# Kernel optimization log

Measured on AMD Instinct MI355X. Metric: run time of the kernel, lower is better.

Reference implementation:

```python
import jax, jax.numpy as jnp
import numpy as np

B, R, N = 4, 1024, 100
REG_FG_THRESH = 0.55
EPS = 1e-8


def _cross2(a, b):
    return a[..., 0] * b[..., 1] - a[..., 1] * b[..., 0]


def _corners_bev(box):
    # box: (7,) [x,y,z,dx,dy,dz,heading] -> (4,2) CCW BEV corners
    x, y, dx, dy, ang = box[0], box[1], box[3], box[4], box[6]
    c, s = jnp.cos(ang), jnp.sin(ang)
    lx = jnp.array([0.5, -0.5, -0.5, 0.5], dtype=box.dtype) * dx
    ly = jnp.array([0.5, 0.5, -0.5, -0.5], dtype=box.dtype) * dy
    return jnp.stack([x + lx * c - ly * s, y + lx * s + ly * c], axis=-1)


def _points_in_box(pts, box):
    # pts (P,2), box (7,) -> (P,) bool; transform into box frame
    c, s = jnp.cos(box[6]), jnp.sin(box[6])
    px = pts[:, 0] - box[0]
    py = pts[:, 1] - box[1]
    lx = px * c + py * s
    ly = -px * s + py * c
    return (jnp.abs(lx) <= box[3] * 0.5 + 1e-5) & (jnp.abs(ly) <= box[4] * 0.5 + 1e-5)


def _bev_inter_area(boxa, boxb):
    # exact rotated-rectangle intersection area (convex polygon of <=8 verts)
    ca = _corners_bev(boxa)
    cb = _corners_bev(boxb)
    in_b = _points_in_box(ca, boxb)
    in_a = _points_in_box(cb, boxa)
    a1, a2 = ca, jnp.roll(ca, -1, axis=0)
    b1, b2 = cb, jnp.roll(cb, -1, axis=0)
    d1 = a2 - a1
    d2 = b2 - b1
    denom = _cross2(d1[:, None, :], d2[None, :, :])              # (4,4)
    diff = b1[None, :, :] - a1[:, None, :]                       # (4,4,2)
    safe = jnp.where(jnp.abs(denom) > EPS, denom, EPS)
    t = _cross2(diff, d2[None, :, :]) / safe
    u = _cross2(diff, d1[:, None, :]) / safe
    hit = (jnp.abs(denom) > EPS) & (t >= 0) & (t <= 1) & (u >= 0) & (u <= 1)
    pin = a1[:, None, :] + t[..., None] * d1[:, None, :]         # (4,4,2)
    pts = jnp.concatenate([ca, cb, pin.reshape(16, 2)], axis=0)  # (24,2)
    val = jnp.concatenate([in_b, in_a, hit.reshape(16)], axis=0)
    nv = val.sum()
    ctr = (pts * val[:, None]).sum(0) / jnp.maximum(nv, 1)
    ang = jnp.where(val, jnp.arctan2(pts[:, 1] - ctr[1], pts[:, 0] - ctr[0]), 1e9)
    order = jnp.argsort(ang)
    p = pts[order]
    v = val[order]
    first = p[0]
    p = jnp.where(v[:, None], p, first)   # pad invalid slots with first vertex (zero shoelace contribution)
    q = jnp.roll(p, -1, axis=0)
    area = 0.5 * jnp.abs(jnp.sum(p[:, 0] * q[:, 1] - q[:, 0] * p[:, 1]))
    return jnp.where(nv >= 3, area, jnp.zeros((), dtype=pts.dtype))


def _iou3d_pair(a, b):
    # same math as iou3d_nms_utils.boxes_iou3d_gpu for one pair
    inter_bev = _bev_inter_area(a, b)
    oh = jnp.clip(jnp.minimum(a[2] + a[5] * 0.5, b[2] + b[5] * 0.5)
                  - jnp.maximum(a[2] - a[5] * 0.5, b[2] - b[5] * 0.5), 0.0)
    inter = inter_bev * oh
    va = a[3] * a[4] * a[5]
    vb = b[3] * b[4] * b[5]
    return inter / jnp.clip(va + vb - inter, 1e-6, None)


_iou_rois_gts = jax.vmap(jax.vmap(_iou3d_pair, in_axes=(None, 0)), in_axes=(0, None))  # (R,N)
_iou_batched = jax.vmap(_iou_rois_gts)                                                  # (B,R,N)


def setup_inputs() -> dict:
    key = jax.random.key(0)
    ks = jax.random.split(key, 9)
    xy = jax.random.uniform(ks[0], (B, N, 2), minval=-40.0, maxval=40.0)
    z = jax.random.uniform(ks[1], (B, N, 1), minval=-2.0, maxval=0.0)
    dims = jax.random.uniform(ks[2], (B, N, 3), minval=1.0, maxval=4.5)
    heading = jax.random.uniform(ks[3], (B, N, 1), minval=-np.pi, maxval=np.pi)
    labels = jax.random.randint(ks[4], (B, N, 1), 1, 4).astype(jnp.float32)
    gt_boxes = jnp.concatenate([xy, z, dims, heading, labels], axis=-1)  # (B,N,8)
    # sampling ROIs are jittered GT boxes, mirroring generate_sampling_roi
    base_idx = jax.random.randint(ks[5], (B, R), 0, N)
    base = jnp.take_along_axis(gt_boxes[..., :7], base_idx[..., None], axis=1)  # (B,R,7)
    ctr_off = jax.random.uniform(ks[6], (B, R, 3), minval=-0.5, maxval=0.5) * base[..., 3:6]
    scale = jax.random.uniform(ks[7], (B, R, 3), minval=0.8, maxval=1.25)
    ang_off = jax.random.uniform(ks[8], (B, R, 1), minval=-np.pi / 4, maxval=np.pi / 4)
    sampling_rois = jnp.concatenate(
        [base[..., :3] + ctr_off, base[..., 3:6] * scale, base[..., 6:7] + ang_off], axis=-1)
    sampling_rois_labels = jnp.take_along_axis(gt_boxes[..., 7], base_idx, axis=1).astype(jnp.int32)
    return {"sampling_rois": sampling_rois,
            "sampling_rois_labels": sampling_rois_labels,
            "gt_boxes": gt_boxes}


def reference(sampling_rois, sampling_rois_labels, gt_boxes):
    # sample_rois_for_rcnn core: all-pairs rotated 3D IoU, best-GT assignment,
    # gather gt_of_rois, then forward()'s reg_valid_mask thresholding.
    iou3d = _iou_batched(sampling_rois, gt_boxes[..., :7])        # (B,R,N)
    max_overlaps = iou3d.max(axis=-1)                             # (B,R)
    gt_assignment = iou3d.argmax(axis=-1)                         # (B,R)
    gt_of_rois = jnp.take_along_axis(gt_boxes, gt_assignment[..., None], axis=1)  # (B,R,8)
    reg_valid_mask = (max_overlaps > REG_FG_THRESH).astype(jnp.int32)
    return sampling_rois, gt_of_rois, max_overlaps, sampling_rois_labels, reg_valid_mask
```

## Files before the change

kernel.cpp:

```cpp
#include <hip/hip_runtime.h>
#include <math.h>

#define BB 4
#define RR 1024
#define NN 100
#define NROI (BB * RR)
#define RPB 2
#define PPB (RPB * NN)
#define NBLK (NROI / RPB)

#define INIT_PACK 0x00000000FFFFFFFFull

__device__ __forceinline__ void corner_of(int i, float cx0, float cy0, float dx, float dy,
                                          float c, float s, float& X, float& Y) {
    float sx = (i == 0 || i == 3) ? 0.5f : -0.5f;
    float sy = (i <= 1) ? 0.5f : -0.5f;
    float lx = sx * dx, ly = sy * dy;
    X = cx0 + lx * c - ly * s;
    Y = cy0 + lx * s + ly * c;
}

__global__ __launch_bounds__(256) void sampling_target_fused(
    const float* __restrict__ rois,
    const int*   __restrict__ labels,
    const float* __restrict__ gts,
    float*       __restrict__ out)
{
    __shared__ int   s_list[PPB];
    __shared__ int   s_cnt;
    __shared__ unsigned long long s_best[RPB];

    const int tid = threadIdx.x;
    const int roi0 = blockIdx.x * RPB;
    const int b = roi0 >> 10;

    if (tid < RPB) s_best[tid] = INIT_PACK;
    if (tid == 0) s_cnt = 0;
    __syncthreads();

    {
        bool hit = false;
        const int p = tid;
        if (p < PPB) {
            int rl = p / NN;
            int n = p - rl * NN;
            const float* A = &rois[(roi0 + rl) * 7];
            const float* G = &gts[(b * NN + n) * 8];
            float oh = fminf(A[2] + A[5] * 0.5f, G[2] + G[5] * 0.5f)
                     - fmaxf(A[2] - A[5] * 0.5f, G[2] - G[5] * 0.5f);
            float dxc = A[0] - G[0], dyc = A[1] - G[1];
            float ra = 0.5f * sqrtf(A[3] * A[3] + A[4] * A[4]);
            float rb = 0.5f * sqrtf(G[3] * G[3] + G[4] * G[4]);
            float rr = ra + rb;
            hit = (oh > 0.0f) && (dxc * dxc + dyc * dyc <= rr * rr);
        }
        unsigned long long m = __ballot(hit);
        int wl = tid & 63;
        int nh = __popcll(m);
        if (nh) {
            int base = 0;
            if (wl == 0) base = atomicAdd(&s_cnt, nh);
            base = __shfl(base, 0, 64);
            if (hit) {
                int pfx = __popcll(m & ((1ull << wl) - 1ull));
                s_list[base + pfx] = p;
            }
        }
    }
    __syncthreads();

    const int cnt = s_cnt;
    const int g = tid >> 5;
    const int lane = tid & 31;
    const int half = g & 1;

    for (int i = g; i < cnt; i += 8) {
        int p = s_list[i];
        int rl = p / NN;
        int n = p - rl * NN;
        const float* A = &rois[(roi0 + rl) * 7];
        const float* G = &gts[(b * NN + n) * 8];
        float ax = A[0], ay = A[1], az = A[2], adx = A[3], ady = A[4], adz = A[5], aang = A[6];
        float gx_ = G[0], gy_ = G[1], gz_ = G[2], gdx = G[3], gdy = G[4], gdz = G[5], gang = G[6];
        float acs = cosf(aang), asn = sinf(aang);
        float bcs = cosf(gang), bsn = sinf(gang);

        float ppx = 0.0f, ppy = 0.0f;
        bool val = false;
        if (lane < 4) {
            corner_of(lane, ax, ay, adx, ady, acs, asn, ppx, ppy);
            float qx = ppx - gx_, qy = ppy - gy_;
            float lx = qx * bcs + qy * bsn;
            float ly = -qx * bsn + qy * bcs;
            val = (fabsf(lx) <= gdx * 0.5f + 1e-5f) && (fabsf(ly) <= gdy * 0.5f + 1e-5f);
        } else if (lane < 8) {
            corner_of(lane - 4, gx_, gy_, gdx, gdy, bcs, bsn, ppx, ppy);
            float qx = ppx - ax, qy = ppy - ay;
            float lx = qx * acs + qy * asn;
            float ly = -qx * asn + qy * acs;
            val = (fabsf(lx) <= adx * 0.5f + 1e-5f) && (fabsf(ly) <= ady * 0.5f + 1e-5f);
        } else if (lane < 24) {
            int e = lane - 8;
            int ii = e >> 2, jj = e & 3;
            float a1x, a1y, a2x, a2y, b1x, b1y, b2x, b2y;
            corner_of(ii, ax, ay, adx, ady, acs, asn, a1x, a1y);
            corner_of((ii + 1) & 3, ax, ay, adx, ady, acs, asn, a2x, a2y);
            corner_of(jj, gx_, gy_, gdx, gdy, bcs, bsn, b1x, b1y);
            corner_of((jj + 1) & 3, gx_, gy_, gdx, gdy, bcs, bsn, b2x, b2y);
            float d1x = a2x - a1x, d1y = a2y - a1y;
            float d2x = b2x - b1x, d2y = b2y - b1y;
            float denom = d1x * d2y - d1y * d2x;
            float fx = b1x - a1x, fy = b1y - a1y;
            float safe = (fabsf(denom) > 1e-8f) ? denom : 1e-8f;
            float t = (fx * d2y - fy * d2x) / safe;
            float u = (fx * d1y - fy * d1x) / safe;
            ppx = a1x + t * d1x;
            ppy = a1y + t * d1y;
            val = (fabsf(denom) > 1e-8f) && (t >= 0.0f) && (t <= 1.0f) && (u >= 0.0f) && (u <= 1.0f);
        }

        unsigned long long m = __ballot(val);
        unsigned gm = (unsigned)(half ? (m >> 32) : (m & 0xFFFFFFFFull));
        int nv = __popc(gm);

        float inter_bev = 0.0f;
        if (nv >= 3) {
            float sx = val ? ppx : 0.0f;
            float sy = val ? ppy : 0.0f;
#pragma unroll
            for (int off = 16; off; off >>= 1) {
                sx += __shfl_xor(sx, off, 32);
                sy += __shfl_xor(sy, off, 32);
            }
            float cx = sx / (float)nv, cy = sy / (float)nv;

            float dxp = ppx - cx, dyp = ppy - cy;
            float den = fabsf(dxp) + fabsf(dyp);
            float pa = dxp / fmaxf(den, 1e-30f);
            float myAng = val ? copysignf(1.0f - pa, dyp) : 1e9f;

            float sAng = 1e30f; int sIdx = 0; bool found = false;
            float gAng = 1e30f; int gIdx = 0;
#pragma unroll
            for (int j = 0; j < 24; j++) {
                float aj = __shfl(myAng, j, 32);
                if (aj < 1e8f) {
                    bool greater = (aj > myAng) || (aj == myAng && j > lane);
                    if (greater && aj < sAng) { sAng = aj; sIdx = j; found = true; }
                    if (aj < gAng) { gAng = aj; gIdx = j; }
                }
            }
            int qi = found ? sIdx : gIdx;
            float qx = __shfl(ppx, qi, 32);
            float qy = __shfl(ppy, qi, 32);
            float contrib = val ? (ppx * qy - qx * ppy) : 0.0f;
#pragma unroll
            for (int off = 16; off; off >>= 1)
                contrib += __shfl_xor(contrib, off, 32);
            inter_bev = 0.5f * fabsf(contrib);
        }

        if (lane == 0) {
            float oh = fminf(az + adz * 0.5f, gz_ + gdz * 0.5f)
                     - fmaxf(az - adz * 0.5f, gz_ - gdz * 0.5f);
            float inter = inter_bev * oh;
            float va = adx * ady * adz;
            float vb = gdx * gdy * gdz;
            float v = inter / fmaxf(va + vb - inter, 1e-6f);
            unsigned long long packed =
                ((unsigned long long)__float_as_uint(v) << 32) | (unsigned)(~(unsigned)n);
            atomicMax(&s_best[rl], packed);
        }
    }
    __syncthreads();

    if (tid < RPB) {
        int r = roi0 + tid;
        unsigned long long packed = s_best[tid];
        float mo = __uint_as_float((unsigned)(packed >> 32));
        int besti = (int)(~(unsigned)(packed & 0xFFFFFFFFu));

        const float* Ar = &rois[r * 7];
        const float* Gb = &gts[(b * NN + besti) * 8];

        float* out_rois = out;
        float* out_gor  = out + NROI * 7;
        float* out_max  = out_gor + NROI * 8;
        float* out_lab  = out_max + NROI;
        float* out_msk  = out_lab + NROI;

#pragma unroll
        for (int k = 0; k < 7; k++) out_rois[r * 7 + k] = Ar[k];
#pragma unroll
        for (int k = 0; k < 8; k++) out_gor[r * 8 + k] = Gb[k];
        out_max[r] = mo;
        out_lab[r] = (float)labels[r];
        out_msk[r] = (mo > 0.55f) ? 1.0f : 0.0f;
    }
}

extern "C" void kernel_launch(void* const* d_in, const int* in_sizes, int n_in,
                              void* d_out, int out_size, void* d_ws, size_t ws_size,
                              hipStream_t stream) {
    const float* rois   = (const float*)d_in[0];
    const int*   labels = (const int*)d_in[1];
    const float* gts    = (const float*)d_in[2];
    float* out = (float*)d_out;

    hipLaunchKernelGGL(sampling_target_fused, dim3(NBLK), dim3(256), 0, stream,
                       rois, labels, gts, out);
}
```

Baseline: 70.32 us.

## Stage GT and ROI boxes with precomputed trig in shared memory, four ROIs per block

Each block now loads the batch's 100 GT boxes and its ROIs into shared memory once, precomputing cos/sin and the circumradius per box. The per-pair prefilter and exact-IoU loops read from LDS instead of repeatedly loading from global memory and recomputing the trig. ROIs per block go from 2 to 4 so the GT staging is shared across more work, with the prefilter looping over the 400 pairs. This halves the block count and adds per-block setup and shared memory use, which reduces parallelism.

```diff
diff --git a/kernel.cpp b/kernel.cpp
--- a/kernel.cpp
+++ b/kernel.cpp
@@ -5,7 +5,7 @@
 #define RR 1024
 #define NN 100
 #define NROI (BB * RR)
-#define RPB 2
+#define RPB 4
 #define PPB (RPB * NN)
 #define NBLK (NROI / RPB)
 
@@ -26,6 +26,10 @@
     const float* __restrict__ gts,
     float*       __restrict__ out)
 {
+    __shared__ float s_gx[NN], s_gy[NN], s_gz[NN], s_gdx[NN], s_gdy[NN], s_gdz[NN],
+                     s_gang[NN], s_glab[NN], s_gc[NN], s_gs[NN], s_grb[NN];
+    __shared__ float s_rx[RPB], s_ry[RPB], s_rz[RPB], s_rdx[RPB], s_rdy[RPB], s_rdz[RPB],
+                     s_rang[RPB], s_rc[RPB], s_rs[RPB], s_rra[RPB];
     __shared__ int   s_list[PPB];
     __shared__ int   s_cnt;
     __shared__ unsigned long long s_best[RPB];
@@ -34,24 +38,39 @@
     const int roi0 = blockIdx.x * RPB;
     const int b = roi0 >> 10;
 
+    if (tid < NN) {
+        const float4* G = (const float4*)&gts[(b * NN + tid) * 8];
+        float4 g0 = G[0];
+        float4 g1 = G[1];
+        s_gx[tid] = g0.x;  s_gy[tid] = g0.y;  s_gz[tid] = g0.z;  s_gdx[tid] = g0.w;
+        s_gdy[tid] = g1.x; s_gdz[tid] = g1.y; s_gang[tid] = g1.z; s_glab[tid] = g1.w;
+        s_gc[tid] = cosf(g1.z);
+        s_gs[tid] = sinf(g1.z);
+        s_grb[tid] = 0.5f * sqrtf(g0.w * g0.w + g1.x * g1.x);
+    } else if (tid < NN + RPB) {
+        int rl = tid - NN;
+        const float* A = &rois[(roi0 + rl) * 7];
+        float ax = A[0], ay = A[1], az = A[2], adx = A[3], ady = A[4], adz = A[5], aang = A[6];
+        s_rx[rl] = ax; s_ry[rl] = ay; s_rz[rl] = az;
+        s_rdx[rl] = adx; s_rdy[rl] = ady; s_rdz[rl] = adz; s_rang[rl] = aang;
+        s_rc[rl] = cosf(aang);
+        s_rs[rl] = sinf(aang);
+        s_rra[rl] = 0.5f * sqrtf(adx * adx + ady * ady);
+    }
     if (tid < RPB) s_best[tid] = INIT_PACK;
     if (tid == 0) s_cnt = 0;
     __syncthreads();
 
-    {
+    for (int p0 = 0; p0 < PPB; p0 += 256) {
+        int p = p0 + tid;
         bool hit = false;
-        const int p = tid;
         if (p < PPB) {
             int rl = p / NN;
             int n = p - rl * NN;
-            const float* A = &rois[(roi0 + rl) * 7];
-            const float* G = &gts[(b * NN + n) * 8];
-            float oh = fminf(A[2] + A[5] * 0.5f, G[2] + G[5] * 0.5f)
-                     - fmaxf(A[2] - A[5] * 0.5f, G[2] - G[5] * 0.5f);
-            float dxc = A[0] - G[0], dyc = A[1] - G[1];
-            float ra = 0.5f * sqrtf(A[3] * A[3] + A[4] * A[4]);
-            float rb = 0.5f * sqrtf(G[3] * G[3] + G[4] * G[4]);
-            float rr = ra + rb;
+            float oh = fminf(s_rz[rl] + s_rdz[rl] * 0.5f, s_gz[n] + s_gdz[n] * 0.5f)
+                     - fmaxf(s_rz[rl] - s_rdz[rl] * 0.5f, s_gz[n] - s_gdz[n] * 0.5f);
+            float dxc = s_rx[rl] - s_gx[n], dyc = s_ry[rl] - s_gy[n];
+            float rr = s_rra[rl] + s_grb[n];
             hit = (oh > 0.0f) && (dxc * dxc + dyc * dyc <= rr * rr);
         }
         unsigned long long m = __ballot(hit);
@@ -78,12 +97,12 @@
         int p = s_list[i];
         int rl = p / NN;
         int n = p - rl * NN;
-        const float* A = &rois[(roi0 + rl) * 7];
-        const float* G = &gts[(b * NN + n) * 8];
-        float ax = A[0], ay = A[1], az = A[2], adx = A[3], ady = A[4], adz = A[5], aang = A[6];
-        float gx_ = G[0], gy_ = G[1], gz_ = G[2], gdx = G[3], gdy = G[4], gdz = G[5], gang = G[6];
-        float acs = cosf(aang), asn = sinf(aang);
-        float bcs = cosf(gang), bsn = sinf(gang);
+        float ax = s_rx[rl], ay = s_ry[rl], az = s_rz[rl];
+        float adx = s_rdx[rl], ady = s_rdy[rl], adz = s_rdz[rl];
+        float acs = s_rc[rl], asn = s_rs[rl];
+        float gx_ = s_gx[n], gy_ = s_gy[n], gz_ = s_gz[n];
+        float gdx = s_gdx[n], gdy = s_gdy[n], gdz = s_gdz[n];
+        float bcs = s_gc[n], bsn = s_gs[n];
 
         float ppx = 0.0f, ppy = 0.0f;
         bool val = false;
@@ -180,19 +199,29 @@
         float mo = __uint_as_float((unsigned)(packed >> 32));
         int besti = (int)(~(unsigned)(packed & 0xFFFFFFFFu));
 
-        const float* Ar = &rois[r * 7];
-        const float* Gb = &gts[(b * NN + besti) * 8];
-
         float* out_rois = out;
         float* out_gor  = out + NROI * 7;
         float* out_max  = out_gor + NROI * 8;
         float* out_lab  = out_max + NROI;
         float* out_msk  = out_lab + NROI;
 
-#pragma unroll
-        for (int k = 0; k < 7; k++) out_rois[r * 7 + k] = Ar[k];
-#pragma unroll
-        for (int k = 0; k < 8; k++) out_gor[r * 8 + k] = Gb[k];
+        out_rois[r * 7 + 0] = s_rx[tid];
+        out_rois[r * 7 + 1] = s_ry[tid];
+        out_rois[r * 7 + 2] = s_rz[tid];
+        out_rois[r * 7 + 3] = s_rdx[tid];
+        out_rois[r * 7 + 4] = s_rdy[tid];
+        out_rois[r * 7 + 5] = s_rdz[tid];
+        out_rois[r * 7 + 6] = s_rang[tid];
+
+        out_gor[r * 8 + 0] = s_gx[besti];
+        out_gor[r * 8 + 1] = s_gy[besti];
+        out_gor[r * 8 + 2] = s_gz[besti];
+        out_gor[r * 8 + 3] = s_gdx[besti];
+        out_gor[r * 8 + 4] = s_gdy[besti];
+        out_gor[r * 8 + 5] = s_gdz[besti];
+        out_gor[r * 8 + 6] = s_gang[besti];
+        out_gor[r * 8 + 7] = s_glab[besti];
+
         out_max[r] = mo;
         out_lab[r] = (float)labels[r];
         out_msk[r] = (mo > 0.55f) ? 1.0f : 0.0f;
```

Measured after the change: 66.26 us. 5.8% less time.

## Assign fixed ROI-half per warp group and iterate hit GTs via ballot bitmask

Applied to the files above, without the earlier changes.

Each 32-lane group now owns one ROI and half of the GT boxes, running the cheap prefilter per lane and then looping over hit bits with shuffles to broadcast GT parameters. This removes the shared-memory hit list, its atomics and one block barrier, and keeps the best IoU in registers instead of using a shared atomicMax. ROIs per block rise from two to four, and GT loads and output copies use float4 accesses. The trade-off is load imbalance between groups, since each group's loop length depends on its own hit count, plus serialized shuffle broadcasts per candidate.

```diff
diff --git a/kernel.cpp b/kernel.cpp
--- a/kernel.cpp
+++ b/kernel.cpp
@@ -5,8 +5,7 @@
 #define RR 1024
 #define NN 100
 #define NROI (BB * RR)
-#define RPB 2
-#define PPB (RPB * NN)
+#define RPB 4
 #define NBLK (NROI / RPB)
 
 #define INIT_PACK 0x00000000FFFFFFFFull
@@ -26,176 +25,178 @@
     const float* __restrict__ gts,
     float*       __restrict__ out)
 {
-    __shared__ int   s_list[PPB];
-    __shared__ int   s_cnt;
-    __shared__ unsigned long long s_best[RPB];
-
-    const int tid = threadIdx.x;
+    __shared__ unsigned long long s_best[8];
+
+    const int tid  = threadIdx.x;
     const int roi0 = blockIdx.x * RPB;
-    const int b = roi0 >> 10;
-
-    if (tid < RPB) s_best[tid] = INIT_PACK;
-    if (tid == 0) s_cnt = 0;
-    __syncthreads();
-
-    {
-        bool hit = false;
-        const int p = tid;
-        if (p < PPB) {
-            int rl = p / NN;
-            int n = p - rl * NN;
-            const float* A = &rois[(roi0 + rl) * 7];
-            const float* G = &gts[(b * NN + n) * 8];
-            float oh = fminf(A[2] + A[5] * 0.5f, G[2] + G[5] * 0.5f)
-                     - fmaxf(A[2] - A[5] * 0.5f, G[2] - G[5] * 0.5f);
-            float dxc = A[0] - G[0], dyc = A[1] - G[1];
-            float ra = 0.5f * sqrtf(A[3] * A[3] + A[4] * A[4]);
-            float rb = 0.5f * sqrtf(G[3] * G[3] + G[4] * G[4]);
-            float rr = ra + rb;
-            hit = (oh > 0.0f) && (dxc * dxc + dyc * dyc <= rr * rr);
-        }
-        unsigned long long m = __ballot(hit);
-        int wl = tid & 63;
-        int nh = __popcll(m);
-        if (nh) {
-            int base = 0;
-            if (wl == 0) base = atomicAdd(&s_cnt, nh);
-            base = __shfl(base, 0, 64);
-            if (hit) {
-                int pfx = __popcll(m & ((1ull << wl) - 1ull));
-                s_list[base + pfx] = p;
-            }
-        }
-    }
-    __syncthreads();
-
-    const int cnt = s_cnt;
-    const int g = tid >> 5;
+    const int b    = roi0 >> 10;
+    const int g    = tid >> 5;
     const int lane = tid & 31;
     const int half = g & 1;
-
-    for (int i = g; i < cnt; i += 8) {
-        int p = s_list[i];
-        int rl = p / NN;
-        int n = p - rl * NN;
-        const float* A = &rois[(roi0 + rl) * 7];
-        const float* G = &gts[(b * NN + n) * 8];
-        float ax = A[0], ay = A[1], az = A[2], adx = A[3], ady = A[4], adz = A[5], aang = A[6];
-        float gx_ = G[0], gy_ = G[1], gz_ = G[2], gdx = G[3], gdy = G[4], gdz = G[5], gang = G[6];
-        float acs = cosf(aang), asn = sinf(aang);
-        float bcs = cosf(gang), bsn = sinf(gang);
-
-        float ppx = 0.0f, ppy = 0.0f;
-        bool val = false;
-        if (lane < 4) {
-            corner_of(lane, ax, ay, adx, ady, acs, asn, ppx, ppy);
-            float qx = ppx - gx_, qy = ppy - gy_;
-            float lx = qx * bcs + qy * bsn;
-            float ly = -qx * bsn + qy * bcs;
-            val = (fabsf(lx) <= gdx * 0.5f + 1e-5f) && (fabsf(ly) <= gdy * 0.5f + 1e-5f);
-        } else if (lane < 8) {
-            corner_of(lane - 4, gx_, gy_, gdx, gdy, bcs, bsn, ppx, ppy);
-            float qx = ppx - ax, qy = ppy - ay;
-            float lx = qx * acs + qy * asn;
-            float ly = -qx * asn + qy * acs;
-            val = (fabsf(lx) <= adx * 0.5f + 1e-5f) && (fabsf(ly) <= ady * 0.5f + 1e-5f);
-        } else if (lane < 24) {
-            int e = lane - 8;
-            int ii = e >> 2, jj = e & 3;
-            float a1x, a1y, a2x, a2y, b1x, b1y, b2x, b2y;
-            corner_of(ii, ax, ay, adx, ady, acs, asn, a1x, a1y);
-            corner_of((ii + 1) & 3, ax, ay, adx, ady, acs, asn, a2x, a2y);
-            corner_of(jj, gx_, gy_, gdx, gdy, bcs, bsn, b1x, b1y);
-            corner_of((jj + 1) & 3, gx_, gy_, gdx, gdy, bcs, bsn, b2x, b2y);
-            float d1x = a2x - a1x, d1y = a2y - a1y;
-            float d2x = b2x - b1x, d2y = b2y - b1y;
-            float denom = d1x * d2y - d1y * d2x;
-            float fx = b1x - a1x, fy = b1y - a1y;
-            float safe = (fabsf(denom) > 1e-8f) ? denom : 1e-8f;
-            float t = (fx * d2y - fy * d2x) / safe;
-            float u = (fx * d1y - fy * d1x) / safe;
-            ppx = a1x + t * d1x;
-            ppy = a1y + t * d1y;
-            val = (fabsf(denom) > 1e-8f) && (t >= 0.0f) && (t <= 1.0f) && (u >= 0.0f) && (u <= 1.0f);
+    const int rl   = g >> 1;
+    const int h    = g & 1;
+    const int r    = roi0 + rl;
+
+    const float* A = &rois[r * 7];
+    float ax = A[0], ay = A[1], az = A[2], adx = A[3], ady = A[4], adz = A[5], aang = A[6];
+    float acs = cosf(aang), asn = sinf(aang);
+    float ra  = 0.5f * sqrtf(adx * adx + ady * ady);
+    float azl = az - adz * 0.5f, azh = az + adz * 0.5f;
+    float va  = adx * ady * adz;
+
+    unsigned long long best = INIT_PACK;
+
+    for (int r2 = 0; r2 < 2; ++r2) {
+        int local = r2 * 32 + lane;
+        int n     = h * 50 + local;
+        bool valid = (local < 50);
+
+        float4 g0 = make_float4(0.f, 0.f, 0.f, 0.f);
+        float4 g1 = make_float4(0.f, 0.f, 0.f, 0.f);
+        if (valid) {
+            const float4* G = (const float4*)&gts[(b * NN + n) * 8];
+            g0 = G[0];
+            g1 = G[1];
         }
-
-        unsigned long long m = __ballot(val);
+        float gc = cosf(g1.z), gs = sinf(g1.z);
+
+        float ohz = fminf(azh, g0.z + g1.y * 0.5f) - fmaxf(azl, g0.z - g1.y * 0.5f);
+        float dxc = ax - g0.x, dyc = ay - g0.y;
+        float rsum = ra + 0.5f * sqrtf(g0.w * g0.w + g1.x * g1.x);
+        bool hit = valid && (ohz > 0.0f) && (dxc * dxc + dyc * dyc <= rsum * rsum);
+
+        unsigned long long m = __ballot(hit);
         unsigned gm = (unsigned)(half ? (m >> 32) : (m & 0xFFFFFFFFull));
-        int nv = __popc(gm);
-
-        float inter_bev = 0.0f;
-        if (nv >= 3) {
-            float sx = val ? ppx : 0.0f;
-            float sy = val ? ppy : 0.0f;
+
+        while (gm) {
+            int j = __ffs(gm) - 1;
+            gm &= gm - 1;
+
+            float gx_ = __shfl(g0.x, j, 32);
+            float gy_ = __shfl(g0.y, j, 32);
+            float gz_ = __shfl(g0.z, j, 32);
+            float gdx = __shfl(g0.w, j, 32);
+            float gdy = __shfl(g1.x, j, 32);
+            float gdz = __shfl(g1.y, j, 32);
+            float bcs = __shfl(gc, j, 32);
+            float bsn = __shfl(gs, j, 32);
+            int   nj  = h * 50 + r2 * 32 + j;
+
+            float ppx = 0.0f, ppy = 0.0f;
+            bool val = false;
+            if (lane < 4) {
+                corner_of(lane, ax, ay, adx, ady, acs, asn, ppx, ppy);
+                float qx = ppx - gx_, qy = ppy - gy_;
+                float lx = qx * bcs + qy * bsn;
+                float ly = -qx * bsn + qy * bcs;
+                val = (fabsf(lx) <= gdx * 0.5f + 1e-5f) && (fabsf(ly) <= gdy * 0.5f + 1e-5f);
+            } else if (lane < 8) {
+                corner_of(lane - 4, gx_, gy_, gdx, gdy, bcs, bsn, ppx, ppy);
+                float qx = ppx - ax, qy = ppy - ay;
+                float lx = qx * acs + qy * asn;
+                float ly = -qx * asn + qy * acs;
+                val = (fabsf(lx) <= adx * 0.5f + 1e-5f) && (fabsf(ly) <= ady * 0.5f + 1e-5f);
+            } else if (lane < 24) {
+                int e = lane - 8;
+                int ii = e >> 2, jj = e & 3;
+                float a1x, a1y, a2x, a2y, b1x, b1y, b2x, b2y;
+                corner_of(ii, ax, ay, adx, ady, acs, asn, a1x, a1y);
+                corner_of((ii + 1) & 3, ax, ay, adx, ady, acs, asn, a2x, a2y);
+                corner_of(jj, gx_, gy_, gdx, gdy, bcs, bsn, b1x, b1y);
+                corner_of((jj + 1) & 3, gx_, gy_, gdx, gdy, bcs, bsn, b2x, b2y);
+                float d1x = a2x - a1x, d1y = a2y - a1y;
+                float d2x = b2x - b1x, d2y = b2y - b1y;
+                float denom = d1x * d2y - d1y * d2x;
+                float fx = b1x - a1x, fy = b1y - a1y;
+                float safe = (fabsf(denom) > 1e-8f) ? denom : 1e-8f;
+                float t = (fx * d2y - fy * d2x) / safe;
+                float u = (fx * d1y - fy * d1x) / safe;
+                ppx = a1x + t * d1x;
+                ppy = a1y + t * d1y;
+                val = (fabsf(denom) > 1e-8f) && (t >= 0.0f) && (t <= 1.0f) && (u >= 0.0f) && (u <= 1.0f);
+            }
+
+            unsigned long long mv = __ballot(val);
+            unsigned gv = (unsigned)(half ? (mv >> 32) : (mv & 0xFFFFFFFFull));
+            int nv = __popc(gv);
+
+            float inter_bev = 0.0f;
+            if (nv >= 3) {
+                float sx = val ? ppx : 0.0f;
+                float sy = val ? ppy : 0.0f;
 #pragma unroll
-            for (int off = 16; off; off >>= 1) {
-                sx += __shfl_xor(sx, off, 32);
-                sy += __shfl_xor(sy, off, 32);
+                for (int off = 16; off; off >>= 1) {
+                    sx += __shfl_xor(sx, off, 32);
+                    sy += __shfl_xor(sy, off, 32);
+                }
+                float cx = sx / (float)nv, cy = sy / (float)nv;
+
+                float dxp = ppx - cx, dyp = ppy - cy;
+                float den = fabsf(dxp) + fabsf(dyp);
+                float pa = dxp / fmaxf(den, 1e-30f);
+                float myAng = val ? copysignf(1.0f - pa, dyp) : 1e9f;
+
+                float sAng = 1e30f; int sIdx = 0; bool found = false;
+                float gAng = 1e30f; int gIdx = 0;
+#pragma unroll
+                for (int jx = 0; jx < 24; jx++) {
+                    float aj = __shfl(myAng, jx, 32);
+                    if (aj < 1e8f) {
+                        bool greater = (aj > myAng) || (aj == myAng && jx > lane);
+                        if (greater && aj < sAng) { sAng = aj; sIdx = jx; found = true; }
+                        if (aj < gAng) { gAng = aj; gIdx = jx; }
+                    }
+                }
+                int qi = found ? sIdx : gIdx;
+                float qx = __shfl(ppx, qi, 32);
+                float qy = __shfl(ppy, qi, 32);
+                float contrib = val ? (ppx * qy - qx * ppy) : 0.0f;
+#pragma unroll
+                for (int off = 16; off; off >>= 1)
+                    contrib += __shfl_xor(contrib, off, 32);
+                inter_bev = 0.5f * fabsf(contrib);
             }
-            float cx = sx / (float)nv, cy = sy / (float)nv;
-
-            float dxp = ppx - cx, dyp = ppy - cy;
-            float den = fabsf(dxp) + fabsf(dyp);
-            float pa = dxp / fmaxf(den, 1e-30f);
-            float myAng = val ? copysignf(1.0f - pa, dyp) : 1e9f;
-
-            float sAng = 1e30f; int sIdx = 0; bool found = false;
-            float gAng = 1e30f; int gIdx = 0;
-#pragma unroll
-            for (int j = 0; j < 24; j++) {
-                float aj = __shfl(myAng, j, 32);
-                if (aj < 1e8f) {
-                    bool greater = (aj > myAng) || (aj == myAng && j > lane);
-                    if (greater && aj < sAng) { sAng = aj; sIdx = j; found = true; }
-                    if (aj < gAng) { gAng = aj; gIdx = j; }
-                }
-            }
-            int qi = found ? sIdx : gIdx;
-            float qx = __shfl(ppx, qi, 32);
-            float qy = __shfl(ppy, qi, 32);
-            float contrib = val ? (ppx * qy - qx * ppy) : 0.0f;
-#pragma unroll
-            for (int off = 16; off; off >>= 1)
-                contrib += __shfl_xor(contrib, off, 32);
-            inter_bev = 0.5f * fabsf(contrib);
-        }
-
-        if (lane == 0) {
-            float oh = fminf(az + adz * 0.5f, gz_ + gdz * 0.5f)
-                     - fmaxf(az - adz * 0.5f, gz_ - gdz * 0.5f);
-            float inter = inter_bev * oh;
-            float va = adx * ady * adz;
+
+            float ohp = fminf(azh, gz_ + gdz * 0.5f) - fmaxf(azl, gz_ - gdz * 0.5f);
+            float inter = inter_bev * ohp;
             float vb = gdx * gdy * gdz;
             float v = inter / fmaxf(va + vb - inter, 1e-6f);
             unsigned long long packed =
-                ((unsigned long long)__float_as_uint(v) << 32) | (unsigned)(~(unsigned)n);
-            atomicMax(&s_best[rl], packed);
+                ((unsigned long long)__float_as_uint(v) << 32) | (unsigned)(~(unsigned)nj);
+            best = (packed > best) ? packed : best;
         }
     }
+
+    if (lane == 0) s_best[g] = best;
     __syncthreads();
 
+    float* out_rois = out;
+    float* out_gor  = out + NROI * 7;
+    float* out_max  = out_gor + NROI * 8;
+    float* out_lab  = out_max + NROI;
+    float* out_msk  = out_lab + NROI;
+
+    if (tid < RPB * 7)
+        out_rois[roi0 * 7 + tid] = rois[roi0 * 7 + tid];
+
     if (tid < RPB) {
-        int r = roi0 + tid;
-        unsigned long long packed = s_best[tid];
+        unsigned long long p0 = s_best[2 * tid];
+        unsigned long long p1 = s_best[2 * tid + 1];
+        unsigned long long packed = (p0 > p1) ? p0 : p1;
         float mo = __uint_as_float((unsigned)(packed >> 32));
         int besti = (int)(~(unsigned)(packed & 0xFFFFFFFFu));
 
-        const float* Ar = &rois[r * 7];
-        const float* Gb = &gts[(b * NN + besti) * 8];
-
-        float* out_rois = out;
-        float* out_gor  = out + NROI * 7;
-        float* out_max  = out_gor + NROI * 8;
-        float* out_lab  = out_max + NROI;
-        float* out_msk  = out_lab + NROI;
-
-#pragma unroll
-        for (int k = 0; k < 7; k++) out_rois[r * 7 + k] = Ar[k];
-#pragma unroll
-        for (int k = 0; k < 8; k++) out_gor[r * 8 + k] = Gb[k];
-        out_max[r] = mo;
-        out_lab[r] = (float)labels[r];
-        out_msk[r] = (mo > 0.55f) ? 1.0f : 0.0f;
+        int rr_ = roi0 + tid;
+        const float4* G = (const float4*)&gts[(b * NN + besti) * 8];
+        float4 q0 = G[0];
+        float4 q1 = G[1];
+        float4* og = (float4*)&out_gor[rr_ * 8];
+        og[0] = q0;
+        og[1] = q1;
+
+        out_max[rr_] = mo;
+        out_lab[rr_] = (float)labels[rr_];
+        out_msk[rr_] = (mo > 0.55f) ? 1.0f : 0.0f;
     }
 }
 
```

Measured after the change: 71.01 us. About the same (+1.0%).

## Stage GT and ROI params with precomputed sin/cos in shared memory, 4 ROIs per block

Applied to the files above, without the earlier changes.

Doubles ROIs per block to 4, so each block has 400 pairs and each thread filters two of them. GT and ROI parameters, including their cos/sin, are staged in shared memory once per block instead of being recomputed per pair in the polygon loop. The global atomic-counter compaction becomes per-wave segments, and the output copies are moved earlier and vectorised with float4. This removes redundant transcendental work and global loads in the hot loop, at the cost of fewer blocks and more shared memory per block.

```diff
diff --git a/kernel.cpp b/kernel.cpp
--- a/kernel.cpp
+++ b/kernel.cpp
@@ -5,9 +5,10 @@
 #define RR 1024
 #define NN 100
 #define NROI (BB * RR)
-#define RPB 2
+#define RPB 4
 #define PPB (RPB * NN)
 #define NBLK (NROI / RPB)
+#define SEGCAP 128
 
 #define INIT_PACK 0x00000000FFFFFFFFull
 
@@ -26,64 +27,120 @@
     const float* __restrict__ gts,
     float*       __restrict__ out)
 {
-    __shared__ int   s_list[PPB];
-    __shared__ int   s_cnt;
+    __shared__ float s_gx[NN], s_gy[NN], s_gz[NN], s_gdx[NN], s_gdy[NN], s_gdz[NN],
+                     s_gc[NN], s_gs[NN];
+    __shared__ float s_rx[RPB], s_ry[RPB], s_rz[RPB], s_rdx[RPB], s_rdy[RPB], s_rdz[RPB],
+                     s_rc[RPB], s_rs[RPB];
+    __shared__ int   s_list[4 * SEGCAP];
+    __shared__ int   s_wcnt[4];
     __shared__ unsigned long long s_best[RPB];
 
-    const int tid = threadIdx.x;
+    const int tid  = threadIdx.x;
+    const int w    = tid >> 6;
+    const int wl   = tid & 63;
     const int roi0 = blockIdx.x * RPB;
-    const int b = roi0 >> 10;
+    const int b    = roi0 >> 10;
+
+    float* out_rois = out;
+    float* out_gor  = out + NROI * 7;
+    float* out_max  = out_gor + NROI * 8;
+    float* out_lab  = out_max + NROI;
+    float* out_msk  = out_lab + NROI;
 
     if (tid < RPB) s_best[tid] = INIT_PACK;
-    if (tid == 0) s_cnt = 0;
-    __syncthreads();
-
+
+    if (tid < RPB * 7) out_rois[roi0 * 7 + tid] = rois[roi0 * 7 + tid];
+    if (tid >= 28 && tid < 28 + RPB) {
+        int rl = tid - 28;
+        out_lab[roi0 + rl] = (float)labels[roi0 + rl];
+    }
+
+    int segbase = 0;
     {
+        const int p  = tid;
+        const int rl = p / NN;
+        const int n  = p - rl * NN;
+        const float4* G = (const float4*)&gts[(b * NN + n) * 8];
+        float4 g0 = G[0];
+        float4 g1 = G[1];
+
+        if (tid < NN) {
+            s_gx[tid] = g0.x;  s_gy[tid] = g0.y;  s_gz[tid] = g0.z;  s_gdx[tid] = g0.w;
+            s_gdy[tid] = g1.x; s_gdz[tid] = g1.y;
+            s_gc[tid] = cosf(g1.z);
+            s_gs[tid] = sinf(g1.z);
+        } else if (tid < NN + RPB) {
+            int rr_ = tid - NN;
+            const float* Ar = &rois[(roi0 + rr_) * 7];
+            s_rx[rr_] = Ar[0]; s_ry[rr_] = Ar[1]; s_rz[rr_] = Ar[2];
+            s_rdx[rr_] = Ar[3]; s_rdy[rr_] = Ar[4]; s_rdz[rr_] = Ar[5];
+            s_rc[rr_] = cosf(Ar[6]);
+            s_rs[rr_] = sinf(Ar[6]);
+        }
+
+        const float* A = &rois[(roi0 + rl) * 7];
+        float oh = fminf(A[2] + A[5] * 0.5f, g0.z + g1.y * 0.5f)
+                 - fmaxf(A[2] - A[5] * 0.5f, g0.z - g1.y * 0.5f);
+        float dxc = A[0] - g0.x, dyc = A[1] - g0.y;
+        float ra = 0.5f * sqrtf(A[3] * A[3] + A[4] * A[4]);
+        float rb = 0.5f * sqrtf(g0.w * g0.w + g1.x * g1.x);
+        float rr = ra + rb;
+        bool hit = (oh > 0.0f) && (dxc * dxc + dyc * dyc <= rr * rr);
+
+        unsigned long long m = __ballot(hit);
+        if (hit) {
+            int pos = __popcll(m & ((1ull << wl) - 1ull));
+            s_list[w * SEGCAP + pos] = p;
+        }
+        segbase = __popcll(m);
+    }
+    {
+        const int p  = tid + 256;
+        const bool inb = (p < PPB);
         bool hit = false;
-        const int p = tid;
-        if (p < PPB) {
-            int rl = p / NN;
-            int n = p - rl * NN;
+        if (inb) {
+            const int rl = p / NN;
+            const int n  = p - rl * NN;
+            const float4* G = (const float4*)&gts[(b * NN + n) * 8];
+            float4 g0 = G[0];
+            float4 g1 = G[1];
             const float* A = &rois[(roi0 + rl) * 7];
-            const float* G = &gts[(b * NN + n) * 8];
-            float oh = fminf(A[2] + A[5] * 0.5f, G[2] + G[5] * 0.5f)
-                     - fmaxf(A[2] - A[5] * 0.5f, G[2] - G[5] * 0.5f);
-            float dxc = A[0] - G[0], dyc = A[1] - G[1];
+            float oh = fminf(A[2] + A[5] * 0.5f, g0.z + g1.y * 0.5f)
+                     - fmaxf(A[2] - A[5] * 0.5f, g0.z - g1.y * 0.5f);
+            float dxc = A[0] - g0.x, dyc = A[1] - g0.y;
             float ra = 0.5f * sqrtf(A[3] * A[3] + A[4] * A[4]);
-            float rb = 0.5f * sqrtf(G[3] * G[3] + G[4] * G[4]);
+            float rb = 0.5f * sqrtf(g0.w * g0.w + g1.x * g1.x);
             float rr = ra + rb;
             hit = (oh > 0.0f) && (dxc * dxc + dyc * dyc <= rr * rr);
         }
         unsigned long long m = __ballot(hit);
-        int wl = tid & 63;
-        int nh = __popcll(m);
-        if (nh) {
-            int base = 0;
-            if (wl == 0) base = atomicAdd(&s_cnt, nh);
-            base = __shfl(base, 0, 64);
-            if (hit) {
-                int pfx = __popcll(m & ((1ull << wl) - 1ull));
-                s_list[base + pfx] = p;
-            }
-        }
+        if (hit) {
+            int pos = __popcll(m & ((1ull << wl) - 1ull));
+            s_list[w * SEGCAP + segbase + pos] = p + 0;
+        }
+        if (wl == 0) s_wcnt[w] = segbase + __popcll(m);
     }
     __syncthreads();
 
-    const int cnt = s_cnt;
-    const int g = tid >> 5;
+    const int c0 = s_wcnt[0], c1 = s_wcnt[1], c2 = s_wcnt[2], c3 = s_wcnt[3];
+    const int p1 = c0, p2 = c0 + c1, p3 = c0 + c1 + c2;
+    const int ct = p3 + c3;
+    const int g    = tid >> 5;
     const int lane = tid & 31;
     const int half = g & 1;
 
-    for (int i = g; i < cnt; i += 8) {
-        int p = s_list[i];
+    for (int i = g; i < ct; i += 8) {
+        int seg = (i >= p1) + (i >= p2) + (i >= p3);
+        int off = (seg == 0) ? 0 : ((seg == 1) ? p1 : ((seg == 2) ? p2 : p3));
+        int p = s_list[seg * SEGCAP + (i - off)];
         int rl = p / NN;
-        int n = p - rl * NN;
-        const float* A = &rois[(roi0 + rl) * 7];
-        const float* G = &gts[(b * NN + n) * 8];
-        float ax = A[0], ay = A[1], az = A[2], adx = A[3], ady = A[4], adz = A[5], aang = A[6];
-        float gx_ = G[0], gy_ = G[1], gz_ = G[2], gdx = G[3], gdy = G[4], gdz = G[5], gang = G[6];
-        float acs = cosf(aang), asn = sinf(aang);
-        float bcs = cosf(gang), bsn = sinf(gang);
+        int n  = p - rl * NN;
+        float ax = s_rx[rl], ay = s_ry[rl], az = s_rz[rl];
+        float adx = s_rdx[rl], ady = s_rdy[rl], adz = s_rdz[rl];
+        float acs = s_rc[rl], asn = s_rs[rl];
+        float gx_ = s_gx[n], gy_ = s_gy[n], gz_ = s_gz[n];
+        float gdx = s_gdx[n], gdy = s_gdy[n], gdz = s_gdz[n];
+        float bcs = s_gc[n], bsn = s_gs[n];
 
         float ppx = 0.0f, ppy = 0.0f;
         bool val = false;
@@ -128,9 +185,9 @@
             float sx = val ? ppx : 0.0f;
             float sy = val ? ppy : 0.0f;
 #pragma unroll
-            for (int off = 16; off; off >>= 1) {
-                sx += __shfl_xor(sx, off, 32);
-                sy += __shfl_xor(sy, off, 32);
+            for (int off2 = 16; off2; off2 >>= 1) {
+                sx += __shfl_xor(sx, off2, 32);
+                sy += __shfl_xor(sy, off2, 32);
             }
             float cx = sx / (float)nv, cy = sy / (float)nv;
 
@@ -142,12 +199,12 @@
             float sAng = 1e30f; int sIdx = 0; bool found = false;
             float gAng = 1e30f; int gIdx = 0;
 #pragma unroll
-            for (int j = 0; j < 24; j++) {
-                float aj = __shfl(myAng, j, 32);
+            for (int jx = 0; jx < 24; jx++) {
+                float aj = __shfl(myAng, jx, 32);
                 if (aj < 1e8f) {
-                    bool greater = (aj > myAng) || (aj == myAng && j > lane);
-                    if (greater && aj < sAng) { sAng = aj; sIdx = j; found = true; }
-                    if (aj < gAng) { gAng = aj; gIdx = j; }
+                    bool greater = (aj > myAng) || (aj == myAng && jx > lane);
+                    if (greater && aj < sAng) { sAng = aj; sIdx = jx; found = true; }
+                    if (aj < gAng) { gAng = aj; gIdx = jx; }
                 }
             }
             int qi = found ? sIdx : gIdx;
@@ -155,8 +212,8 @@
             float qy = __shfl(ppy, qi, 32);
             float contrib = val ? (ppx * qy - qx * ppy) : 0.0f;
 #pragma unroll
-            for (int off = 16; off; off >>= 1)
-                contrib += __shfl_xor(contrib, off, 32);
+            for (int off2 = 16; off2; off2 >>= 1)
+                contrib += __shfl_xor(contrib, off2, 32);
             inter_bev = 0.5f * fabsf(contrib);
         }
 
@@ -180,21 +237,14 @@
         float mo = __uint_as_float((unsigned)(packed >> 32));
         int besti = (int)(~(unsigned)(packed & 0xFFFFFFFFu));
 
-        const float* Ar = &rois[r * 7];
-        const float* Gb = &gts[(b * NN + besti) * 8];
-
-        float* out_rois = out;
-        float* out_gor  = out + NROI * 7;
-        float* out_max  = out_gor + NROI * 8;
-        float* out_lab  = out_max + NROI;
-        float* out_msk  = out_lab + NROI;
-
-#pragma unroll
-        for (int k = 0; k < 7; k++) out_rois[r * 7 + k] = Ar[k];
-#pragma unroll
-        for (int k = 0; k < 8; k++) out_gor[r * 8 + k] = Gb[k];
+        const float4* G = (const float4*)&gts[(b * NN + besti) * 8];
+        float4 q0 = G[0];
+        float4 q1 = G[1];
+        float4* og = (float4*)&out_gor[r * 8];
+        og[0] = q0;
+        og[1] = q1;
+
         out_max[r] = mo;
-        out_lab[r] = (float)labels[r];
         out_msk[r] = (mo > 0.55f) ? 1.0f : 0.0f;
     }
 }
```

New measurement: 66.37 us. 5.6% less time.
